# Performance work log

Measured on AMD Instinct MI355X. Metric: run time of the kernel, lower is better.

Reference implementation:

```python
import jax, jax.numpy as jnp
import numpy as np
from jax import lax

N, D, M, H = 8192, 32, 8, 128
ATOL = 1e-5
RTOL = 1e-5
MAX_STEPS = 10   # bounded adaptive dopri5 iterations (accept/reject with masking)
DT0 = 0.25


def setup_inputs() -> dict:
    key = jax.random.key(0)
    ks = jax.random.split(key, 6)
    p = lambda k, shape, s: jax.random.normal(k, shape, jnp.float32) * s
    return {
        "z": jax.random.normal(ks[0], (N, D), jnp.float32),
        "G_w": p(ks[1], (M, D), 0.3),
        "W1": p(ks[2], (H, D), (1.0 / D) ** 0.5),
        "b1": jnp.zeros((H,), jnp.float32),
        "W2": p(ks[3], (H, H), (1.0 / H) ** 0.5),
        "b2": jnp.zeros((H,), jnp.float32),
        "W3": p(ks[4], (D, H), (1.0 / H) ** 0.5),
        "b3": jnp.zeros((D,), jnp.float32),
        "T": jnp.ones((1,), jnp.float32),
    }


def qpnf_forward(z, G_w, W1, b1, W2, b2, W3, b3, T):
    d = z.shape[1]

    def mlp(x):  # dF network: d -> 128 -> 128 -> d
        h = jax.nn.relu(x @ W1.T + b1)
        h = jax.nn.relu(h @ W2.T + b2)
        return h @ W3.T + b3

    # G is linear (no bias) so jacrev(G)(x) == G_w for every sample; the batched
    # dG @ dG^T solves collapse to one shared (m,m) solve / (d,d) projector.
    A = G_w @ G_w.T                       # (m, m)
    AinvG = jnp.linalg.solve(A, G_w)      # (m, d) = A^{-1} W
    P = G_w.T @ AinvG                     # (d, d) null-space projector W^T A^{-1} W
    IP = jnp.eye(d, dtype=z.dtype) - P
    trP = jnp.trace(P)

    jac_mlp = jax.vmap(jax.jacrev(lambda xi: mlp(xi[None, :])[0]))  # (N,d,d)

    def f(y):  # augmented state y = [x | logp], dlogp/dt = -div(dx/dx)
        x = y[:, :d]
        dF = mlp(x)                        # (N, d)
        g = x @ G_w.T                      # (N, m)
        dz = -(dF @ IP) - g @ AinvG        # -(eta_J) - (eta_C)
        JdF = jac_mlp(x)                   # (N, d, d)
        # J_f = -(I-P) JdF - P  ->  dlogp = -trace(J_f)
        dlogp = jnp.einsum('jk,nkj->n', IP, JdF) + trP
        return jnp.concatenate([dz, dlogp[:, None]], axis=1)

    def rk_step(y, dt):  # Dormand-Prince 5(4)
        k1 = f(y)
        k2 = f(y + dt * (0.2 * k1))
        k3 = f(y + dt * (3/40 * k1 + 9/40 * k2))
        k4 = f(y + dt * (44/45 * k1 - 56/15 * k2 + 32/9 * k3))
        k5 = f(y + dt * (19372/6561 * k1 - 25360/2187 * k2 + 64448/6561 * k3 - 212/729 * k4))
        k6 = f(y + dt * (9017/3168 * k1 - 355/33 * k2 + 46732/5247 * k3 + 49/176 * k4 - 5103/18656 * k5))
        y1 = y + dt * (35/384 * k1 + 500/1113 * k3 + 125/192 * k4 - 2187/6784 * k5 + 11/84 * k6)
        k7 = f(y1)
        err = dt * ((35/384 - 5179/57600) * k1 + (500/1113 - 7571/16695) * k3
                    + (125/192 - 393/640) * k4 + (-2187/6784 + 92097/339200) * k5
                    + (11/84 - 187/2100) * k6 - (1/40) * k7)
        return y1, err

    t1 = 2.0 * T[0]  # eval path: integration_times[-1] *= 2
    y0 = jnp.concatenate([z, jnp.zeros((z.shape[0], 1), z.dtype)], axis=1)

    def body(carry, _):
        t, dt, y = carry
        done = t >= t1 - 1e-9
        dtc = jnp.where(done, jnp.asarray(1e-3, z.dtype), jnp.minimum(dt, t1 - t))
        y1, ev = rk_step(y, dtc)
        tol = ATOL + RTOL * jnp.maximum(jnp.abs(y), jnp.abs(y1))
        errn = jnp.sqrt(jnp.mean((ev / tol) ** 2))
        accept = jnp.logical_and(~done, errn <= 1.0)
        y_new = jnp.where(accept, y1, y)
        t_new = jnp.where(accept, t + dtc, t)
        factor = jnp.clip(0.9 * errn ** (-0.2), 0.2, 10.0)
        dt_new = jnp.where(done, dt, jnp.clip(dtc * factor, 1e-6, t1))
        dt_new = lax.stop_gradient(dt_new)
        return (t_new, dt_new, y_new), None

    init = (jnp.asarray(0.0, z.dtype), jnp.asarray(DT0, z.dtype), y0)
    (_, _, yT), _ = lax.scan(body, init, None, length=MAX_STEPS)
    return yT[:, :d]


def reference(z, G_w, W1, b1, W2, b2, W3, b3, T):
    return qpnf_forward(z, G_w, W1, b1, W2, b2, W3, b3, T)
```

## Files before the change

kernel.cpp:

```cpp
#include <hip/hip_runtime.h>
#include <hip/hip_cooperative_groups.h>
#include <math.h>

namespace cg = cooperative_groups;
typedef float4 f4;
typedef float2 f2;
typedef float v2f __attribute__((ext_vector_type(2)));

#define NT 512
#define RB 32

#define WS_WR    0
#define WS_PART  32768
#define WS_TOTAL 35328

#define L_W1T   0
#define L_C3T   4096
#define L_PT    8320
#define L_XW    9472
#define L_H1W   10496
#define L_H2W   14592
#define L_H1M   18688
#define L_KZ    22784
#define L_KL    30848
#define L_YZ    31072
#define L_Y1Z   32224
#define L_YL    33376
#define L_Y1L   33408
#define L_B1    33440
#define L_B2    33568
#define L_C0    33696
#define L_GS    33728
#define L_AAUG  33984
#define L_AINVG 34112
#define L_MISC  34368
#define LDS_FLOATS 34372
#define L_RED   L_H1W
#define L_P     L_H2W
#define L_IP    (L_H2W + 1024)
#define L_IPW3  L_KZ

__device__ const float ACO[5][5] = {
  { 0.2f, 0.f, 0.f, 0.f, 0.f },
  { (float)(3.0/40.0), (float)(9.0/40.0), 0.f, 0.f, 0.f },
  { (float)(44.0/45.0), (float)(-56.0/15.0), (float)(32.0/9.0), 0.f, 0.f },
  { (float)(19372.0/6561.0), (float)(-25360.0/2187.0), (float)(64448.0/6561.0), (float)(-212.0/729.0), 0.f },
  { (float)(9017.0/3168.0), (float)(-355.0/33.0), (float)(46732.0/5247.0), (float)(49.0/176.0), (float)(-5103.0/18656.0) }
};

#define B1C ((float)(35.0/384.0))
#define B3C ((float)(500.0/1113.0))
#define B4C ((float)(125.0/192.0))
#define B5C ((float)(-2187.0/6784.0))
#define B6C ((float)(11.0/84.0))

#define E1C ((float)(35.0/384.0 - 5179.0/57600.0))
#define E3C ((float)(500.0/1113.0 - 7571.0/16695.0))
#define E4C ((float)(125.0/192.0 - 393.0/640.0))
#define E5C ((float)(-2187.0/6784.0 + 92097.0/339200.0))
#define E6C ((float)(11.0/84.0 - 187.0/2100.0))
#define E7C ((float)(-1.0/40.0))

__device__ __forceinline__ f4 ld4(const float* p){ return *(const f4*)p; }
__device__ __forceinline__ void st4(float* p, f4 v){ *(f4*)p = v; }

__device__ __forceinline__ void pk_lo(v2f& d, v2f s, v2f b){
  asm("v_pk_fma_f32 %0, %1, %2, %0 op_sel:[0,0,0] op_sel_hi:[0,1,1]"
      : "+v"(d) : "v"(s), "v"(b));
}
__device__ __forceinline__ void pk_hi(v2f& d, v2f s, v2f b){
  asm("v_pk_fma_f32 %0, %1, %2, %0 op_sel:[1,0,0] op_sel_hi:[1,1,1]"
      : "+v"(d) : "v"(s), "v"(b));
}
__device__ __forceinline__ v2f vlo(f4 v){ v2f r; r.x = v.x; r.y = v.y; return r; }
__device__ __forceinline__ v2f vhi(f4 v){ v2f r; r.x = v.z; r.y = v.w; return r; }

__device__ __forceinline__ void assemble_x(float* lds, int tid, float dtc,
                                           const float* co, int np)
{
  const int w = tid >> 6, lane = tid & 63;
  const int r = lane >> 4;
  const int c = (lane << 1) & 31;
  const int o = (4 * w + r) * 36 + c;
  f2 y = *(const f2*)&lds[L_YZ + o];
  float sx = 0.f, sy = 0.f;
  for (int p = 0; p < np; p++){
    f2 kv = *(const f2*)&lds[L_KZ + p * 1152 + o];
    sx += co[p] * kv.x; sy += co[p] * kv.y;
  }
  float* XWp = &lds[L_XW + w * 128];
  XWp[(c + 0) * 4 + r] = y.x + dtc * sx;
  XWp[(c + 1) * 4 + r] = y.y + dtc * sy;
}

__device__ void eval_f(float* lds, const float* __restrict__ ws, int tid,
                       float trP, int kout)
{
  const int w = tid >> 6, lane = tid & 63;
  const int cg = lane & 31, kh = lane >> 5;
  float* XWp = &lds[L_XW  + w * 128];
  float* H1p = &lds[L_H1W + w * 512];
  float* H2p = &lds[L_H2W + w * 512];
  float* H1m = &lds[L_H1M + w * 512];

  const f4* WR4 = (const f4*)&ws[WS_WR];
  const int kb = kh * 64;
  f4 wb[4], rb[4];
#pragma unroll
  for (int u = 0; u < 4; u++){
    wb[u] = WR4[(kb + u) * 64 + cg];
    rb[u] = WR4[(kb + u) * 64 + 32 + cg];
  }

  v2f a12[4][2];
#pragma unroll
  for (int i = 0; i < 4; i++)
#pragma unroll
    for (int jp = 0; jp < 2; jp++){ a12[i][jp].x = 0.f; a12[i][jp].y = 0.f; }
#pragma unroll 4
  for (int t = 0; t < 16; t++){
    const int k = kh * 16 + t;
    f4 xv = ld4(&XWp[k * 4]);
    f4 wv = ld4(&lds[L_W1T + k * 128 + 4 * cg]);
    v2f x0 = vlo(xv), x1 = vhi(xv);
    v2f wA = vlo(wv), wB = vhi(wv);
    pk_lo(a12[0][0], wA, x0); pk_lo(a12[0][1], wA, x1);
    pk_hi(a12[1][0], wA, x0); pk_hi(a12[1][1], wA, x1);
    pk_lo(a12[2][0], wB, x0); pk_lo(a12[2][1], wB, x1);
    pk_hi(a12[3][0], wB, x0); pk_hi(a12[3][1], wB, x1);
  }
  float a1s[4][4];
#pragma unroll
  for (int i = 0; i < 4; i++){
    a1s[i][0] = a12[i][0].x; a1s[i][1] = a12[i][0].y;
    a1s[i][2] = a12[i][1].x; a1s[i][3] = a12[i][1].y;
  }
#pragma unroll
  for (int i = 0; i < 4; i++)
#pragma unroll
    for (int j = 0; j < 4; j++) a1s[i][j] += __shfl_xor(a1s[i][j], 32);
  if (kh == 0){
    f4 b1v = ld4(&lds[L_B1 + 4 * cg]);
    const float* b1p = (const float*)&b1v;
#pragma unroll
    for (int i = 0; i < 4; i++){
      f4 hv; float* hp = (float*)&hv;
      f4 mv; float* mp = (float*)&mv;
#pragma unroll
      for (int j = 0; j < 4; j++){
        float pre = a1s[i][j] + b1p[i];
        hp[j] = fmaxf(pre, 0.f);
        mp[j] = (pre > 0.f) ? 1.f : 0.f;
      }
      st4(&H1p[(4 * cg + i) * 4], hv);
      st4(&H1m[(4 * cg + i) * 4], mv);
    }
  }

  v2f ah2[4][2], at2[4][2];
#pragma unroll
  for (int i = 0; i < 4; i++)
#pragma unroll
    for (int jp = 0; jp < 2; jp++){
      ah2[i][jp].x = 0.f; ah2[i][jp].y = 0.f;
      at2[i][jp].x = 0.f; at2[i][jp].y = 0.f;
    }
#pragma unroll 1
  for (int g = 0; g < 16; g++){
    f4 wc[4], rc[4];
#pragma unroll
    for (int u = 0; u < 4; u++){ wc[u] = wb[u]; rc[u] = rb[u]; }
    if (g < 15){
      const int kn = kb + (g + 1) * 4;
#pragma unroll
      for (int u = 0; u < 4; u++){
        wb[u] = WR4[(kn + u) * 64 + cg];
        rb[u] = WR4[(kn + u) * 64 + 32 + cg];
      }
    }
#pragma unroll
    for (int u = 0; u < 4; u++){
      const int k = kb + g * 4 + u;
      f4 av = ld4(&H1p[k * 4]);
      f4 mv = ld4(&H1m[k * 4]);
      v2f a0 = vlo(av), a1 = vhi(av);
      v2f m0 = vlo(mv), m1 = vhi(mv);
      v2f wA = vlo(wc[u]), wB = vhi(wc[u]);
      v2f rA = vlo(rc[u]), rB = vhi(rc[u]);
      pk_lo(ah2[0][0], wA, a0); pk_lo(ah2[0][1], wA, a1);
      pk_hi(ah2[1][0], wA, a0); pk_hi(ah2[1][1], wA, a1);
      pk_lo(ah2[2][0], wB, a0); pk_lo(ah2[2][1], wB, a1);
      pk_hi(ah2[3][0], wB, a0); pk_hi(ah2[3][1], wB, a1);
      pk_lo(at2[0][0], rA, m0); pk_lo(at2[0][1], rA, m1);
      pk_hi(at2[1][0], rA, m0); pk_hi(at2[1][1], rA, m1);
      pk_lo(at2[2][0], rB, m0); pk_lo(at2[2][1], rB, m1);
      pk_hi(at2[3][0], rB, m0); pk_hi(at2[3][1], rB, m1);
    }
  }
  float ah[4][4], at[4][4];
#pragma unroll
  for (int i = 0; i < 4; i++){
    ah[i][0] = ah2[i][0].x; ah[i][1] = ah2[i][0].y;
    ah[i][2] = ah2[i][1].x; ah[i][3] = ah2[i][1].y;
    at[i][0] = at2[i][0].x; at[i][1] = at2[i][0].y;
    at[i][2] = at2[i][1].x; at[i][3] = at2[i][1].y;
  }
#pragma unroll
  for (int i = 0; i < 4; i++)
#pragma unroll
    for (int j = 0; j < 4; j++){
      ah[i][j] += __shfl_xor(ah[i][j], 32);
      at[i][j] += __shfl_xor(at[i][j], 32);
    }

  f4 b2v = ld4(&lds[L_B2 + 4 * cg]);
  const float* b2p = (const float*)&b2v;
  float h2v[4][4]; float dl[4] = {0.f, 0.f, 0.f, 0.f};
#pragma unroll
  for (int i = 0; i < 4; i++)
#pragma unroll
    for (int j = 0; j < 4; j++){
      float pre = ah[i][j] + b2p[i];
      float hv = fmaxf(pre, 0.f);
      h2v[i][j] = hv;
      if (pre > 0.f) dl[j] += at[i][j];
    }
#pragma unroll
  for (int mk = 1; mk < 32; mk <<= 1){
#pragma unroll
    for (int j = 0; j < 4; j++) dl[j] += __shfl_xor(dl[j], mk, 64);
  }
  if (kh == 0){
#pragma unroll
    for (int i = 0; i < 4; i++){
      f4 hv; float* hp = (float*)&hv;
#pragma unroll
      for (int j = 0; j < 4; j++) hp[j] = h2v[i][j];
      st4(&H2p[(4 * cg + i) * 4], hv);
    }
    if (cg == 0){
#pragma unroll
      for (int j = 0; j < 4; j++)
        lds[L_KL + kout * 32 + 4 * w + j] = dl[j] + trP;
    }
  }

  v2f a3e[2], a3o[2];
  a3e[0].x=0.f;a3e[0].y=0.f;a3e[1].x=0.f;a3e[1].y=0.f;
  a3o[0].x=0.f;a3o[0].y=0.f;a3o[1].x=0.f;a3o[1].y=0.f;
  const int bb = kh * 64;
#pragma unroll 4
  for (int t = 0; t < 16; t++){
    f4 cv = ld4(&lds[L_C3T + cg * 132 + bb + 4 * t]);
    v2f cA = vlo(cv), cB = vhi(cv);
    { f4 av = ld4(&H2p[(bb + 4 * t + 0) * 4]);
      pk_lo(a3e[0], cA, vlo(av)); pk_lo(a3e[1], cA, vhi(av)); }
    { f4 av = ld4(&H2p[(bb + 4 * t + 1) * 4]);
      pk_hi(a3o[0], cA, vlo(av)); pk_hi(a3o[1], cA, vhi(av)); }
    { f4 av = ld4(&H2p[(bb + 4 * t + 2) * 4]);
      pk_lo(a3e[0], cB, vlo(av)); pk_lo(a3e[1], cB, vhi(av)); }
    { f4 av = ld4(&H2p[(bb + 4 * t + 3) * 4]);
      pk_hi(a3o[0], cB, vlo(av)); pk_hi(a3o[1], cB, vhi(av)); }
  }
  const int qq = kh * 16;
#pragma unroll
  for (int t = 0; t < 4; t++){
    f4 pv = ld4(&lds[L_PT + cg * 36 + qq + 4 * t]);
    v2f pA = vlo(pv), pB = vhi(pv);
    { f4 av = ld4(&XWp[(qq + 4 * t + 0) * 4]);
      pk_lo(a3e[0], pA, vlo(av)); pk_lo(a3e[1], pA, vhi(av)); }
    { f4 av = ld4(&XWp[(qq + 4 * t + 1) * 4]);
      pk_hi(a3o[0], pA, vlo(av)); pk_hi(a3o[1], pA, vhi(av)); }
    { f4 av = ld4(&XWp[(qq + 4 * t + 2) * 4]);
      pk_lo(a3e[0], pB, vlo(av)); pk_lo(a3e[1], pB, vhi(av)); }
    { f4 av = ld4(&XWp[(qq + 4 * t + 3) * 4]);
      pk_hi(a3o[0], pB, vlo(av)); pk_hi(a3o[1], pB, vhi(av)); }
  }
  float a3[4];
  a3[0] = a3e[0].x + a3o[0].x; a3[1] = a3e[0].y + a3o[0].y;
  a3[2] = a3e[1].x + a3o[1].x; a3[3] = a3e[1].y + a3o[1].y;
#pragma unroll
  for (int j = 0; j < 4; j++) a3[j] += __shfl_xor(a3[j], 32);
  if (kh == 0){
    float c0v = lds[L_C0 + cg];
#pragma unroll
    for (int j = 0; j < 4; j++)
      lds[L_KZ + kout * 1152 + (4 * w + j) * 36 + cg] = -(a3[j] + c0v);
  }
}

__global__ void __launch_bounds__(NT, 2)
qpnf_kernel(const float* __restrict__ z, const float* __restrict__ Gw,
            const float* __restrict__ W1g, const float* __restrict__ b1g,
            const float* __restrict__ W2g, const float* __restrict__ b2g,
            const float* __restrict__ W3g, const float* __restrict__ b3g,
            const float* __restrict__ Tg, float* __restrict__ out,
            float* __restrict__ ws)
{
  __shared__ float lds[LDS_FLOATS];
  const int tid = threadIdx.x;
  const int bid = blockIdx.x;
  const int r0 = bid * RB;
  cg::grid_group grid = cg::this_grid();

  for (int i = 0; i < 8; i++){
    int idx = tid + i * NT;
    int h = idx >> 5, j = idx & 31;
    lds[L_W1T + j * 128 + h] = W1g[idx];
  }
  if (tid < 128){ lds[L_B1 + tid] = b1g[tid]; lds[L_B2 + tid] = b2g[tid]; }
  if (tid < 256) lds[L_GS + tid] = Gw[tid];
  __syncthreads();

  if (tid < 64){
    int i = tid >> 3, j = tid & 7;
    float s = 0.f;
    for (int k = 0; k < 32; k++) s += lds[L_GS + i * 32 + k] * lds[L_GS + j * 32 + k];
    lds[L_AAUG + i * 16 + j] = s;
    lds[L_AAUG + i * 16 + 8 + j] = (i == j) ? 1.f : 0.f;
  }
  __syncthreads();
  if (tid == 0){
    float* A = &lds[L_AAUG];
    for (int c = 0; c < 8; c++){
      int p = c; float mx = fabsf(A[c * 16 + c]);
      for (int r = c + 1; r < 8; r++){
        float v = fabsf(A[r * 16 + c]);
        if (v > mx){ mx = v; p = r; }
      }
      if (p != c)
        for (int q = 0; q < 16; q++){ float t = A[c*16+q]; A[c*16+q] = A[p*16+q]; A[p*16+q] = t; }
      float pv = 1.0f / A[c * 16 + c];
      for (int q = 0; q < 16; q++) A[c * 16 + q] *= pv;
      for (int r = 0; r < 8; r++) if (r != c){
        float fct = A[r * 16 + c];
        for (int q = 0; q < 16; q++) A[r * 16 + q] -= fct * A[c * 16 + q];
      }
    }
  }
  __syncthreads();
  if (tid < 256){
    int m = tid >> 5, d = tid & 31;
    float s = 0.f;
    for (int q = 0; q < 8; q++) s += lds[L_AAUG + m * 16 + 8 + q] * lds[L_GS + q * 32 + d];
    lds[L_AINVG + m * 32 + d] = s;
  }
  __syncthreads();
  for (int i4 = 0; i4 < 2; i4++){
    int idx = tid + i4 * NT;
    int i = idx >> 5, j = idx & 31;
    float s = 0.f;
    for (int m = 0; m < 8; m++) s += lds[L_GS + m * 32 + i] * lds[L_AINVG + m * 32 + j];
    lds[L_P + i * 32 + j] = s;
  }
  __syncthreads();
  float* IPl = &lds[L_IP];
  for (int i4 = 0; i4 < 2; i4++){
    int idx = tid + i4 * NT;
    int i = idx >> 5, j = idx & 31;
    IPl[i * 32 + j] = ((i == j) ? 1.f : 0.f) - lds[L_P + i * 32 + j];
  }
  if (tid == 0){
    float s = 0.f;
    for (int i = 0; i < 32; i++) s += lds[L_P + i * 32 + i];
    lds[L_MISC] = s;
  }
  __syncthreads();
  for (int i4 = 0; i4 < 8; i4++){
    int idx = tid + i4 * NT;
    int b = idx & 127, c = idx >> 7;
    float s = 0.f;
    for (int i = 0; i < 32; i++) s += W3g[i * 128 + b] * IPl[i * 32 + c];
    lds[L_C3T + c * 132 + b] = s;
  }
  for (int i4 = 0; i4 < 2; i4++){
    int idx = tid + i4 * NT;
    int c = idx >> 5, q = idx & 31;
    lds[L_PT + c * 36 + q] = lds[L_P + q * 32 + c];
  }
  if (tid < 32){
    float s = 0.f;
    for (int i = 0; i < 32; i++) s += b3g[i] * IPl[i * 32 + tid];
    lds[L_C0 + tid] = s;
  }
  for (int i4 = 0; i4 < 8; i4++){
    int idx = tid + i4 * NT;
    int j = idx >> 7, b = idx & 127;
    float s = 0.f;
    for (int k = 0; k < 32; k++) s += IPl[j * 32 + k] * W3g[k * 128 + b];
    lds[L_IPW3 + j * 128 + b] = s;
  }
  __syncthreads();
  if (bid < 128 && tid < 128){
    int a = bid;
    float s = 0.f;
    for (int j = 0; j < 32; j++) s += W1g[a * 32 + j] * lds[L_IPW3 + j * 128 + tid];
    ws[WS_WR + a * 256 + 128 + tid] = s * W2g[tid * 128 + a];
  }
  if (bid >= 128 && tid < 128){
    int a = bid - 128;
    ws[WS_WR + a * 256 + tid] = W2g[tid * 128 + a];
  }
  if (tid < 256){
    const int r = tid >> 3, jj = (tid & 7) * 4;
    st4(&lds[L_YZ + r * 36 + jj], ld4(&z[(r0 + r) * 32 + jj]));
  }
  if (tid < RB) lds[L_YL + tid] = 0.f;

  const float trP = lds[L_MISC];
  const float t1 = 2.0f * Tg[0];

  grid.sync();

  float t_cur = 0.f, dt_cur = 0.25f;
  bool prev_acc = false;

  for (int step = 0; step < 10; step++){
    if (t_cur >= t1 - 1e-9f) break;
    const float dtc = fminf(dt_cur, t1 - t_cur);

    for (int s = 1; s <= 6; s++){
      if (s == 1 && step > 0){
        if (prev_acc){
          const int w = tid >> 6, lane = tid & 63;
          const int r = lane >> 4, c = (lane << 1) & 31;
          const int o = (4 * w + r) * 36 + c;
          *(f2*)&lds[L_KZ + o] = *(const f2*)&lds[L_KZ + 6 * 1152 + o];
          if (lane < 4) lds[L_KL + 4 * w + lane] = lds[L_KL + 6 * 32 + 4 * w + lane];
        }
        continue;
      }
      assemble_x(lds, tid, dtc, ACO[s >= 2 ? s - 2 : 0], s - 1);
      eval_f(lds, ws, tid, trP, s - 1);
    }

    __syncthreads();
    if (tid < 256){
      const int r = tid >> 3, jj = (tid & 7) * 4;
      const int o = r * 36 + jj;
      f4 y   = ld4(&lds[L_YZ + o]);
      f4 k1v = ld4(&lds[L_KZ + 0 * 1152 + o]);
      f4 k3v = ld4(&lds[L_KZ + 2 * 1152 + o]);
      f4 k4v = ld4(&lds[L_KZ + 3 * 1152 + o]);
      f4 k5v = ld4(&lds[L_KZ + 4 * 1152 + o]);
      f4 k6v = ld4(&lds[L_KZ + 5 * 1152 + o]);
      f4 x;
      x.x = y.x + dtc * (B1C*k1v.x + B3C*k3v.x + B4C*k4v.x + B5C*k5v.x + B6C*k6v.x);
      x.y = y.y + dtc * (B1C*k1v.y + B3C*k3v.y + B4C*k4v.y + B5C*k5v.y + B6C*k6v.y);
      x.z = y.z + dtc * (B1C*k1v.z + B3C*k3v.z + B4C*k4v.z + B5C*k5v.z + B6C*k6v.z);
      x.w = y.w + dtc * (B1C*k1v.w + B3C*k3v.w + B4C*k4v.w + B5C*k5v.w + B6C*k6v.w);
      st4(&lds[L_Y1Z + o], x);
      float* XWp = &lds[L_XW + (r >> 2) * 128];
      const int rr = r & 3;
      XWp[(jj + 0) * 4 + rr] = x.x;
      XWp[(jj + 1) * 4 + rr] = x.y;
      XWp[(jj + 2) * 4 + rr] = x.z;
      XWp[(jj + 3) * 4 + rr] = x.w;
    }
    if (tid < RB){
      float s = B1C * lds[L_KL + 0*32 + tid] + B3C * lds[L_KL + 2*32 + tid]
              + B4C * lds[L_KL + 3*32 + tid] + B5C * lds[L_KL + 4*32 + tid]
              + B6C * lds[L_KL + 5*32 + tid];
      lds[L_Y1L + tid] = lds[L_YL + tid] + dtc * s;
    }
    __syncthreads();
    eval_f(lds, ws, tid, trP, 6);
    __syncthreads();

    float sacc = 0.f;
    if (tid < 256){
      const int r = tid >> 3, jj = (tid & 7) * 4;
      const int o = r * 36 + jj;
      f4 k1v = ld4(&lds[L_KZ + 0 * 1152 + o]);
      f4 k3v = ld4(&lds[L_KZ + 2 * 1152 + o]);
      f4 k4v = ld4(&lds[L_KZ + 3 * 1152 + o]);
      f4 k5v = ld4(&lds[L_KZ + 4 * 1152 + o]);
      f4 k6v = ld4(&lds[L_KZ + 5 * 1152 + o]);
      f4 k7v = ld4(&lds[L_KZ + 6 * 1152 + o]);
      f4 yv  = ld4(&lds[L_YZ + o]);
      f4 y1v = ld4(&lds[L_Y1Z + o]);
      float ev, tol, q;
      ev = dtc * (E1C*k1v.x + E3C*k3v.x + E4C*k4v.x + E5C*k5v.x + E6C*k6v.x + E7C*k7v.x);
      tol = 1e-5f + 1e-5f * fmaxf(fabsf(yv.x), fabsf(y1v.x)); q = ev / tol; sacc += q * q;
      ev = dtc * (E1C*k1v.y + E3C*k3v.y + E4C*k4v.y + E5C*k5v.y + E6C*k6v.y + E7C*k7v.y);
      tol = 1e-5f + 1e-5f * fmaxf(fabsf(yv.y), fabsf(y1v.y)); q = ev / tol; sacc += q * q;
      ev = dtc * (E1C*k1v.z + E3C*k3v.z + E4C*k4v.z + E5C*k5v.z + E6C*k6v.z + E7C*k7v.z);
      tol = 1e-5f + 1e-5f * fmaxf(fabsf(yv.z), fabsf(y1v.z)); q = ev / tol; sacc += q * q;
      ev = dtc * (E1C*k1v.w + E3C*k3v.w + E4C*k4v.w + E5C*k5v.w + E6C*k6v.w + E7C*k7v.w);
      tol = 1e-5f + 1e-5f * fmaxf(fabsf(yv.w), fabsf(y1v.w)); q = ev / tol; sacc += q * q;
    }
    if (tid < RB){
      float evl = dtc * (E1C * lds[L_KL + 0*32 + tid] + E3C * lds[L_KL + 2*32 + tid]
                + E4C * lds[L_KL + 3*32 + tid] + E5C * lds[L_KL + 4*32 + tid]
                + E6C * lds[L_KL + 5*32 + tid] + E7C * lds[L_KL + 6*32 + tid]);
      float toll = 1e-5f + 1e-5f * fmaxf(fabsf(lds[L_YL + tid]), fabsf(lds[L_Y1L + tid]));
      float ql = evl / toll; sacc += ql * ql;
    }
#pragma unroll
    for (int mk = 1; mk < 64; mk <<= 1) sacc += __shfl_xor(sacc, mk, 64);
    if ((tid & 63) == 0) lds[L_RED + (tid >> 6)] = sacc;
    __syncthreads();
    if (tid == 0){
      float s = lds[L_RED+0] + lds[L_RED+1] + lds[L_RED+2] + lds[L_RED+3]
              + lds[L_RED+4] + lds[L_RED+5] + lds[L_RED+6] + lds[L_RED+7];
      ws[WS_PART + step * 256 + bid] = s;
    }

    grid.sync();

    float ps = 0.f;
    if (tid < 256) ps = ws[WS_PART + step * 256 + tid];
#pragma unroll
    for (int mk = 1; mk < 64; mk <<= 1) ps += __shfl_xor(ps, mk, 64);
    if (tid < 256 && (tid & 63) == 0) lds[L_RED + (tid >> 6)] = ps;
    __syncthreads();
    const float errn = sqrtf((lds[L_RED+0] + lds[L_RED+1] + lds[L_RED+2] + lds[L_RED+3])
                             / 270336.0f);
    __syncthreads();

    const bool accept = (errn <= 1.0f);
    if (accept){
      const int w = tid >> 6, lane = tid & 63;
      const int r = lane >> 4, c = (lane << 1) & 31;
      const int o = (4 * w + r) * 36 + c;
      *(f2*)&lds[L_YZ + o] = *(const f2*)&lds[L_Y1Z + o];
      if (lane < 4) lds[L_YL + 4 * w + lane] = lds[L_Y1L + 4 * w + lane];
      t_cur += dtc;
    }
    float fac = 0.9f * powf(errn, -0.2f);
    fac = fminf(fmaxf(fac, 0.2f), 10.0f);
    dt_cur = fminf(fmaxf(dtc * fac, 1e-6f), t1);
    prev_acc = accept;
  }

  __syncthreads();
  if (tid < 256){
    const int r = tid >> 3, jj = (tid & 7) * 4;
    st4(&out[(r0 + r) * 32 + jj], ld4(&lds[L_YZ + r * 36 + jj]));
  }
}

extern "C" void kernel_launch(void* const* d_in, const int* in_sizes, int n_in,
                              void* d_out, int out_size, void* d_ws, size_t ws_size,
                              hipStream_t stream)
{
  (void)in_sizes; (void)n_in; (void)out_size;
  const float* z  = (const float*)d_in[0];
  const float* Gw = (const float*)d_in[1];
  const float* W1 = (const float*)d_in[2];
  const float* b1 = (const float*)d_in[3];
  const float* W2 = (const float*)d_in[4];
  const float* b2 = (const float*)d_in[5];
  const float* W3 = (const float*)d_in[6];
  const float* b3 = (const float*)d_in[7];
  const float* T  = (const float*)d_in[8];
  float* out = (float*)d_out;
  float* ws  = (float*)d_ws;
  if (ws_size < (size_t)WS_TOTAL * sizeof(float)) return;

  void* args[] = { (void*)&z, (void*)&Gw, (void*)&W1, (void*)&b1, (void*)&W2,
                   (void*)&b2, (void*)&W3, (void*)&b3, (void*)&T, (void*)&out,
                   (void*)&ws };
  hipLaunchCooperativeKernel((const void*)qpnf_kernel, dim3(256), dim3(NT),
                             args, 0, stream);
}
```

Baseline: 1.199 ms.

## Recompute ReLU mask from H1, double-buffer weight prefetch, stagger per-wave start

Removes the separate H1 mask buffer from LDS and recomputes the ReLU mask from the stored activations, cutting one LDS store and one LDS load per element and shrinking the LDS footprint. The global weight prefetch becomes two buffers deep, so loads are issued two groups ahead. Odd waves start at a rotated group offset so neighbouring waves read different weight rows at the same time. This costs extra registers for the second prefetch buffer and a few compare/select instructions per element.

New measurement: 1.330 ms. 10.9% more time.

```diff
diff --git a/kernel.cpp b/kernel.cpp
--- a/kernel.cpp
+++ b/kernel.cpp
@@ -20,21 +20,20 @@
 #define L_XW    9472
 #define L_H1W   10496
 #define L_H2W   14592
-#define L_H1M   18688
-#define L_KZ    22784
-#define L_KL    30848
-#define L_YZ    31072
-#define L_Y1Z   32224
-#define L_YL    33376
-#define L_Y1L   33408
-#define L_B1    33440
-#define L_B2    33568
-#define L_C0    33696
-#define L_GS    33728
-#define L_AAUG  33984
-#define L_AINVG 34112
-#define L_MISC  34368
-#define LDS_FLOATS 34372
+#define L_KZ    18688
+#define L_KL    26752
+#define L_YZ    26976
+#define L_Y1Z   28128
+#define L_YL    29280
+#define L_Y1L   29312
+#define L_B1    29344
+#define L_B2    29472
+#define L_C0    29600
+#define L_GS    29632
+#define L_AAUG  29888
+#define L_AINVG 30016
+#define L_MISC  30272
+#define LDS_FLOATS 30276
 #define L_RED   L_H1W
 #define L_P     L_H2W
 #define L_IP    (L_H2W + 1024)
@@ -101,15 +100,21 @@
   float* XWp = &lds[L_XW  + w * 128];
   float* H1p = &lds[L_H1W + w * 512];
   float* H2p = &lds[L_H2W + w * 512];
-  float* H1m = &lds[L_H1M + w * 512];
 
   const f4* WR4 = (const f4*)&ws[WS_WR];
   const int kb = kh * 64;
-  f4 wb[4], rb[4];
-#pragma unroll
-  for (int u = 0; u < 4; u++){
-    wb[u] = WR4[(kb + u) * 64 + cg];
-    rb[u] = WR4[(kb + u) * 64 + 32 + cg];
+  const int grot = (w & 1) << 3;
+  f4 wbA[4], rbA[4], wbB[4], rbB[4];
+  {
+    const int kA = kb + grot * 4;
+    const int kB = kb + (grot + 1) * 4;
+#pragma unroll
+    for (int u = 0; u < 4; u++){
+      wbA[u] = WR4[(kA + u) * 64 + cg];
+      rbA[u] = WR4[(kA + u) * 64 + 32 + cg];
+      wbB[u] = WR4[(kB + u) * 64 + cg];
+      rbB[u] = WR4[(kB + u) * 64 + 32 + cg];
+    }
   }
 
   v2f a12[4][2];
@@ -145,15 +150,12 @@
 #pragma unroll
     for (int i = 0; i < 4; i++){
       f4 hv; float* hp = (float*)&hv;
-      f4 mv; float* mp = (float*)&mv;
 #pragma unroll
       for (int j = 0; j < 4; j++){
         float pre = a1s[i][j] + b1p[i];
         hp[j] = fmaxf(pre, 0.f);
-        mp[j] = (pre > 0.f) ? 1.f : 0.f;
       }
       st4(&H1p[(4 * cg + i) * 4], hv);
-      st4(&H1m[(4 * cg + i) * 4], mv);
     }
   }
 
@@ -166,35 +168,70 @@
       at2[i][jp].x = 0.f; at2[i][jp].y = 0.f;
     }
 #pragma unroll 1
-  for (int g = 0; g < 16; g++){
-    f4 wc[4], rc[4];
-#pragma unroll
-    for (int u = 0; u < 4; u++){ wc[u] = wb[u]; rc[u] = rb[u]; }
-    if (g < 15){
-      const int kn = kb + (g + 1) * 4;
+  for (int gp = 0; gp < 8; gp++){
+    {
+      f4 wc[4], rc[4];
+#pragma unroll
+      for (int u = 0; u < 4; u++){ wc[u] = wbA[u]; rc[u] = rbA[u]; }
+      if (gp < 7){
+        const int kn = kb + (((2 * gp + 2) + grot) & 15) * 4;
+#pragma unroll
+        for (int u = 0; u < 4; u++){
+          wbA[u] = WR4[(kn + u) * 64 + cg];
+          rbA[u] = WR4[(kn + u) * 64 + 32 + cg];
+        }
+      }
+      const int kc = kb + ((2 * gp + grot) & 15) * 4;
 #pragma unroll
       for (int u = 0; u < 4; u++){
-        wb[u] = WR4[(kn + u) * 64 + cg];
-        rb[u] = WR4[(kn + u) * 64 + 32 + cg];
-      }
-    }
-#pragma unroll
-    for (int u = 0; u < 4; u++){
-      const int k = kb + g * 4 + u;
-      f4 av = ld4(&H1p[k * 4]);
-      f4 mv = ld4(&H1m[k * 4]);
-      v2f a0 = vlo(av), a1 = vhi(av);
-      v2f m0 = vlo(mv), m1 = vhi(mv);
-      v2f wA = vlo(wc[u]), wB = vhi(wc[u]);
-      v2f rA = vlo(rc[u]), rB = vhi(rc[u]);
-      pk_lo(ah2[0][0], wA, a0); pk_lo(ah2[0][1], wA, a1);
-      pk_hi(ah2[1][0], wA, a0); pk_hi(ah2[1][1], wA, a1);
-      pk_lo(ah2[2][0], wB, a0); pk_lo(ah2[2][1], wB, a1);
-      pk_hi(ah2[3][0], wB, a0); pk_hi(ah2[3][1], wB, a1);
-      pk_lo(at2[0][0], rA, m0); pk_lo(at2[0][1], rA, m1);
-      pk_hi(at2[1][0], rA, m0); pk_hi(at2[1][1], rA, m1);
-      pk_lo(at2[2][0], rB, m0); pk_lo(at2[2][1], rB, m1);
-      pk_hi(at2[3][0], rB, m0); pk_hi(at2[3][1], rB, m1);
+        f4 av = ld4(&H1p[(kc + u) * 4]);
+        v2f a0 = vlo(av), a1 = vhi(av);
+        v2f m0, m1;
+        m0.x = (a0.x > 0.f) ? 1.f : 0.f; m0.y = (a0.y > 0.f) ? 1.f : 0.f;
+        m1.x = (a1.x > 0.f) ? 1.f : 0.f; m1.y = (a1.y > 0.f) ? 1.f : 0.f;
+        v2f wA = vlo(wc[u]), wB = vhi(wc[u]);
+        v2f rA = vlo(rc[u]), rB = vhi(rc[u]);
+        pk_lo(ah2[0][0], wA, a0); pk_lo(ah2[0][1], wA, a1);
+        pk_hi(ah2[1][0], wA, a0); pk_hi(ah2[1][1], wA, a1);
+        pk_lo(ah2[2][0], wB, a0); pk_lo(ah2[2][1], wB, a1);
+        pk_hi(ah2[3][0], wB, a0); pk_hi(ah2[3][1], wB, a1);
+        pk_lo(at2[0][0], rA, m0); pk_lo(at2[0][1], rA, m1);
+        pk_hi(at2[1][0], rA, m0); pk_hi(at2[1][1], rA, m1);
+        pk_lo(at2[2][0], rB, m0); pk_lo(at2[2][1], rB, m1);
+        pk_hi(at2[3][0], rB, m0); pk_hi(at2[3][1], rB, m1);
+      }
+    }
+    {
+      f4 wc[4], rc[4];
+#pragma unroll
+      for (int u = 0; u < 4; u++){ wc[u] = wbB[u]; rc[u] = rbB[u]; }
+      if (gp < 7){
+        const int kn = kb + (((2 * gp + 3) + grot) & 15) * 4;
+#pragma unroll
+        for (int u = 0; u < 4; u++){
+          wbB[u] = WR4[(kn + u) * 64 + cg];
+          rbB[u] = WR4[(kn + u) * 64 + 32 + cg];
+        }
+      }
+      const int kc = kb + (((2 * gp + 1) + grot) & 15) * 4;
+#pragma unroll
+      for (int u = 0; u < 4; u++){
+        f4 av = ld4(&H1p[(kc + u) * 4]);
+        v2f a0 = vlo(av), a1 = vhi(av);
+        v2f m0, m1;
+        m0.x = (a0.x > 0.f) ? 1.f : 0.f; m0.y = (a0.y > 0.f) ? 1.f : 0.f;
+        m1.x = (a1.x > 0.f) ? 1.f : 0.f; m1.y = (a1.y > 0.f) ? 1.f : 0.f;
+        v2f wA = vlo(wc[u]), wB = vhi(wc[u]);
+        v2f rA = vlo(rc[u]), rB = vhi(rc[u]);
+        pk_lo(ah2[0][0], wA, a0); pk_lo(ah2[0][1], wA, a1);
+        pk_hi(ah2[1][0], wA, a0); pk_hi(ah2[1][1], wA, a1);
+        pk_lo(ah2[2][0], wB, a0); pk_lo(ah2[2][1], wB, a1);
+        pk_hi(ah2[3][0], wB, a0); pk_hi(ah2[3][1], wB, a1);
+        pk_lo(at2[0][0], rA, m0); pk_lo(at2[0][1], rA, m1);
+        pk_hi(at2[1][0], rA, m0); pk_hi(at2[1][1], rA, m1);
+        pk_lo(at2[2][0], rB, m0); pk_lo(at2[2][1], rB, m1);
+        pk_hi(at2[3][0], rB, m0); pk_hi(at2[3][1], rB, m1);
+      }
     }
   }
   float ah[4][4], at[4][4];
```
